# Kernel optimization log

Measured on AMD Instinct MI355X. Metric: run time of the kernel, lower is better.

Reference implementation:

```python
import jax, jax.numpy as jnp
import numpy as np

FILTER_SIZE = 256          # nperseg and conv kernel length
REG = 1e-7
B, C, T = 512, 8, 6000


def welch_psd(x, nperseg):
    # x: [B, C, T]; window=None (rect), fs=1, noverlap=nperseg//2, detrend by segment mean
    noverlap = nperseg // 2
    step = nperseg - noverlap
    num_seg = (x.shape[-1] - noverlap) // step
    idx = jnp.arange(nperseg)[None, :] + step * jnp.arange(num_seg)[:, None]  # [S, nperseg]
    seg = x[..., idx]                                   # [B, C, S, nperseg]
    seg = seg - seg.mean(axis=-1, keepdims=True)
    fft = jnp.fft.rfft(seg, axis=-1)                    # [B, C, S, F]
    psd = jnp.abs(fft) ** 2 / float(nperseg)
    # one-sided scaling: double all bins except DC (and Nyquist for even nperseg)
    if nperseg % 2 == 0:
        psd = psd.at[..., 1:-1].multiply(2.0)
    else:
        psd = psd.at[..., 1:].multiply(2.0)
    return psd.mean(axis=-2)                            # [B, C, F]


def setup_inputs() -> dict:
    key = jax.random.key(0)
    x = jax.random.normal(key, (B, C, T), dtype=jnp.float32)
    return {"x": x}


def reference(x):
    K = FILTER_SIZE
    n_chan = x.shape[1]
    # center
    x = x - x.mean(axis=-1, keepdims=True)
    psd = welch_psd(x, K) + REG                         # [B, C, F]
    F = psd.shape[-1]
    # barycenter (training, first_iter=True): weights = 1/F elementwise, sum over batch, squared; detached
    new_bary = jnp.sum(jnp.sqrt(psd) / F, axis=0) ** 2  # [C, F]
    target = jax.lax.stop_gradient(new_bary)
    # whitening/mapping filter in frequency domain
    D = jnp.sqrt(target)[None] / jnp.sqrt(psd)          # [B, C, F]
    H = jnp.fft.irfft(D, n=K, axis=-1)                  # [B, C, K]
    H = jnp.fft.fftshift(H, axes=-1)
    H = jnp.flip(H, axis=-1)
    # per-sample depthwise conv1d, padding='same' (torch: left=(K-1)//2, right=K//2 for stride 1)
    lp = (K - 1) // 2
    rp = (K - 1) - lp
    def dw(xb, hb):  # xb: [C, T], hb: [C, K]
        return jax.lax.conv_general_dilated(
            xb[None], hb[:, None, :], (1,), [(lp, rp)],
            feature_group_count=n_chan,
            dimension_numbers=("NCH", "OIH", "NCH"))[0]
    return jax.vmap(dw)(x, H)                           # [B, C, T]
```

## Files before the change

### kernel.cpp

```cpp
#include <hip/hip_runtime.h>
#include <math.h>

#define T_LEN 6000
#define NROWS 4096
#define NCH 8
#define F_BINS 129
#define CF (NCH*F_BINS)
#define NSLOT 16
#define REG_EPS 1e-7f

typedef _Float16 half8 __attribute__((ext_vector_type(8)));
typedef _Float16 half4_t __attribute__((ext_vector_type(4)));
typedef float f32x4 __attribute__((ext_vector_type(4)));

#define PSD_ROWS 8
__global__ __launch_bounds__(512, 2) void psd_kernel(const float* __restrict__ x,
                                                     float* __restrict__ psd,
                                                     float* __restrict__ means,
                                                     float* __restrict__ ssumN) {
  int tid = threadIdx.x;
  int lane = tid & 63;
  int w = tid >> 6;
  int l15 = lane & 15, l4 = lane >> 4;
  __shared__ __align__(16) _Float16 xh[2][6272];
  __shared__ float colsum[256];
  __shared__ float rowm[3][8];

  half8 bf[2][8];
  #pragma unroll
  for (int i = 0; i < 2; ++i) {
    int n = 16 * (2 * w + i) + l15;
    int nn = (n < 129) ? n : (n - 128);
    for (int kk = 0; kk < 8; ++kk) {
      half8 hb;
      for (int e = 0; e < 8; ++e) {
        int k = 32 * kk + 8 * l4 + e;
        float ang = (float)((nn * k) & 255) * (6.283185307179586f / 256.f);
        float s, c;
        __sincosf(ang, &s, &c);
        hb[e] = (_Float16)((n < 129) ? c : s);
      }
      bf[i][kk] = hb;
    }
  }

  int r0 = blockIdx.x * PSD_ROWS;
  float* myslot = ssumN + (size_t)(blockIdx.x & (NSLOT - 1)) * CF;
  float4 v[4];
  {
    const float* xr = x + (size_t)r0 * T_LEN;
    #pragma unroll
    for (int j = 0; j < 4; ++j) {
      int c = tid + 512 * j;
      v[j] = (c < 1500) ? ((const float4*)xr)[c] : make_float4(0.f, 0.f, 0.f, 0.f);
    }
    float rs = 0.f;
    #pragma unroll
    for (int j = 0; j < 4; ++j) {
      int c = tid + 512 * j;
      if (c < 1568) {
        float4 q = v[j];
        rs += q.x + q.y + q.z + q.w;
        half4_t h = { (_Float16)q.x, (_Float16)q.y, (_Float16)q.z, (_Float16)q.w };
        int byte = 8 * c;
        byte ^= ((byte >> 8) & 7) << 4;
        *(half4_t*)((char*)xh[0] + byte) = h;
      }
    }
    #pragma unroll
    for (int off = 32; off >= 1; off >>= 1) rs += __shfl_xor(rs, off);
    if (lane == 0) rowm[0][w] = rs;
    const float* x1 = x + (size_t)(r0 + 1) * T_LEN;
    #pragma unroll
    for (int j = 0; j < 4; ++j) {
      int c = tid + 512 * j;
      v[j] = (c < 1500) ? ((const float4*)x1)[c] : make_float4(0.f, 0.f, 0.f, 0.f);
    }
  }
  __syncthreads();

  for (int jr = 0; jr < PSD_ROWS; ++jr) {
    int r = r0 + jr;
    const char* xcur = (const char*)xh[jr & 1];
    if (jr + 1 < PSD_ROWS) {
      char* xnxt = (char*)xh[(jr + 1) & 1];
      float rs = 0.f;
      #pragma unroll
      for (int j = 0; j < 4; ++j) {
        int c = tid + 512 * j;
        if (c < 1568) {
          float4 q = v[j];
          rs += q.x + q.y + q.z + q.w;
          half4_t h = { (_Float16)q.x, (_Float16)q.y, (_Float16)q.z, (_Float16)q.w };
          int byte = 8 * c;
          byte ^= ((byte >> 8) & 7) << 4;
          *(half4_t*)(xnxt + byte) = h;
        }
      }
      if (jr + 2 < PSD_ROWS) {
        const float* xn = x + (size_t)(r + 2) * T_LEN;
        #pragma unroll
        for (int j = 0; j < 4; ++j) {
          int c = tid + 512 * j;
          v[j] = (c < 1500) ? ((const float4*)xn)[c] : make_float4(0.f, 0.f, 0.f, 0.f);
        }
      }
      #pragma unroll
      for (int off = 32; off >= 1; off >>= 1) rs += __shfl_xor(rs, off);
      if (lane == 0) rowm[(jr + 1) % 3][w] = rs;
    }
    f32x4 acc[2][3];
    #pragma unroll
    for (int i = 0; i < 2; ++i)
      #pragma unroll
      for (int mt = 0; mt < 3; ++mt)
        acc[i][mt] = (f32x4){0.f, 0.f, 0.f, 0.f};
    #pragma unroll
    for (int kk = 0; kk < 8; ++kk) {
      half8 a[3];
      #pragma unroll
      for (int mt = 0; mt < 3; ++mt) {
        int ab = 4096 * mt + 256 * l15 + 64 * kk + 16 * l4;
        ab ^= ((ab >> 8) & 7) << 4;
        a[mt] = *(const half8*)(xcur + ab);
      }
      #pragma unroll
      for (int mt = 0; mt < 3; ++mt) {
        acc[0][mt] = __builtin_amdgcn_mfma_f32_16x16x32_f16(a[mt], bf[0][kk], acc[0][mt], 0, 0, 0);
        acc[1][mt] = __builtin_amdgcn_mfma_f32_16x16x32_f16(a[mt], bf[1][kk], acc[1][mt], 0, 0, 0);
      }
    }
    float s0, s1;
    #pragma unroll
    for (int i = 0; i < 2; ++i) {
      float t = 0.f;
      #pragma unroll
      for (int j = 0; j < 4; ++j) {
        t += acc[i][0][j] * acc[i][0][j];
        t += acc[i][1][j] * acc[i][1][j];
        if (4 * l4 + j < 13) t += acc[i][2][j] * acc[i][2][j];
      }
      t += __shfl_xor(t, 16);
      t += __shfl_xor(t, 32);
      if (i == 0) s0 = t; else s1 = t;
    }
    __syncthreads();
    if (l4 == 0) {
      colsum[16 * (2 * w + 0) + l15] = s0;
      colsum[16 * (2 * w + 1) + l15] = s1;
    }
    __syncthreads();
    if (tid < F_BINS) {
      float vv;
      if (tid == 0) vv = 0.f;
      else if (tid == 128) vv = colsum[128] * (1.f / 11520.f);
      else vv = (colsum[tid] + colsum[tid + 128]) * (1.f / 5760.f);
      float p = vv + REG_EPS;
      psd[(size_t)r * F_BINS + tid] = p;
      atomicAdd(&myslot[jr * F_BINS + tid], sqrtf(p) * (1.f / (float)F_BINS));
    }
    if (tid == 0) {
      float ms = 0.f;
      #pragma unroll
      for (int q = 0; q < 8; ++q) ms += rowm[jr % 3][q];
      means[r] = ms * (1.f / (float)T_LEN);
    }
  }
}

#define BSTRIDE 296
__global__ __launch_bounds__(512) void conv_kernel(const float* __restrict__ x,
                                                   const float* __restrict__ means,
                                                   const float* __restrict__ psd,
                                                   const float* __restrict__ ssumN,
                                                   float* __restrict__ y) {
  int rc = blockIdx.x;
  int c = rc & (NCH - 1);
  int tid = threadIdx.x;
  int lane = tid & 63;
  int w = tid >> 6;
  __shared__ __align__(16) char smem[24576];
  _Float16* xh = (_Float16*)smem;
  _Float16* Bp = (_Float16*)(smem + 13056);
  float* part = (float*)(smem + 13056);
  float* dv = (float*)(smem + 22528);
  float* hv = (float*)(smem + 23044);
  const float* xr = x + (size_t)rc * T_LEN;
  float mean = means[rc];
  if (tid < F_BINS) {
    float s = 0.f;
    #pragma unroll
    for (int p = 0; p < NSLOT; ++p)
      s += ssumN[(size_t)p * CF + c * F_BINS + tid];
    dv[tid] = s * rsqrtf(psd[(size_t)rc * F_BINS + tid]);
  }
  #pragma unroll
  for (int j = 0; j < 4; ++j) {
    int q = tid + 512 * j;
    if (q < 1632) {
      int cc = q - 32;
      half4_t h;
      if (cc >= 0 && cc < 1500) {
        float4 vv = ((const float4*)xr)[cc];
        h = (half4_t){ (_Float16)(vv.x - mean), (_Float16)(vv.y - mean),
                       (_Float16)(vv.z - mean), (_Float16)(vv.w - mean) };
      } else {
        h = (half4_t){ (_Float16)0.f, (_Float16)0.f, (_Float16)0.f, (_Float16)0.f };
      }
      *(half4_t*)((char*)xh + 8 * q) = h;
    }
  }
  __syncthreads();
  if (tid < 258) {
    int t = tid >> 1, p = tid & 1;
    int k0 = p ? 64 : 1;
    int nk = p ? 64 : 63;
    float stc, sts;
    __sincosf((float)t * (6.283185307179586f / 256.f), &sts, &stc);
    float cr, ci;
    __sincosf((float)((t * k0) & 255) * (6.283185307179586f / 256.f), &ci, &cr);
    float acc = 0.f;
    for (int q = 0; q < nk; ++q) {
      acc = fmaf(dv[k0 + q], cr, acc);
      float nr = cr * stc - ci * sts;
      ci = cr * sts + ci * stc;
      cr = nr;
    }
    part[tid] = acc;
  }
  __syncthreads();
  if (tid < F_BINS) {
    float val = dv[0] + ((tid & 1) ? -dv[128] : dv[128]) +
                2.f * (part[2 * tid] + part[2 * tid + 1]);
    hv[tid] = val * (1.f / 256.f);
  }
  __syncthreads();
  #pragma unroll
  for (int j = 0; j < 3; ++j) {
    int idx = tid + 512 * j;
    if (idx < 1152) {
      int n = idx & 15;
      int qq = idx >> 4;
      int s0 = 4 * qq - n - 1;
      half4_t h;
      #pragma unroll
      for (int e = 0; e < 4; ++e) {
        int s = s0 + e;
        float hvv = 0.f;
        if (s >= 0 && s < 256) {
          int ii = s - 127; if (ii < 0) ii = -ii;
          hvv = hv[ii];
        }
        h[e] = (_Float16)hvv;
      }
      *(half4_t*)((char*)Bp + (size_t)n * (2 * BSTRIDE) + 8 * qq) = h;
    }
  }
  __syncthreads();

  int l15 = lane & 15, l4 = lane >> 4;
  f32x4 acc0 = {0.f,0.f,0.f,0.f}, acc1 = {0.f,0.f,0.f,0.f}, acc2 = {0.f,0.f,0.f,0.f};
  const _Float16* bbase = &Bp[BSTRIDE * l15 + 8 * l4];
  const _Float16* abase = &xh[16 * l15 + 8 * l4 + 768 * w];
  #pragma unroll
  for (int kk = 0; kk < 9; ++kk) {
    half8 b = *(const half8*)(bbase + 32 * kk);
    half8 a0 = *(const half8*)(abase + 32 * kk);
    half8 a1 = *(const half8*)(abase + 256 + 32 * kk);
    half8 a2 = *(const half8*)(abase + 512 + 32 * kk);
    acc0 = __builtin_amdgcn_mfma_f32_16x16x32_f16(a0, b, acc0, 0, 0, 0);
    acc1 = __builtin_amdgcn_mfma_f32_16x16x32_f16(a1, b, acc1, 0, 0, 0);
    acc2 = __builtin_amdgcn_mfma_f32_16x16x32_f16(a2, b, acc2, 0, 0, 0);
  }
  __syncthreads();
  float* bw = (float*)smem + 768 * w;
  #pragma unroll
  for (int i = 0; i < 3; ++i) {
    f32x4 a = (i == 0) ? acc0 : (i == 1) ? acc1 : acc2;
    #pragma unroll
    for (int j = 0; j < 4; ++j)
      bw[256 * i + 64 * l4 + 16 * j + l15] = a[j];
  }
  float* yr = y + (size_t)rc * T_LEN + 768 * w;
  const float4* b4 = (const float4*)bw;
  #pragma unroll
  for (int cc = 0; cc < 3; ++cc) {
    int fi = 768 * w + 256 * cc + 4 * lane;
    if (fi < T_LEN)
      *(float4*)&yr[256 * cc + 4 * lane] = b4[64 * cc + lane];
  }
}

extern "C" void kernel_launch(void* const* d_in, const int* in_sizes, int n_in,
                              void* d_out, int out_size, void* d_ws, size_t ws_size,
                              hipStream_t stream) {
  const float* x = (const float*)d_in[0];
  float* out = (float*)d_out;
  float* psd   = (float*)d_ws;
  float* ssumN = psd + (size_t)NROWS * F_BINS;
  float* means = ssumN + (size_t)NSLOT * CF;
  hipMemsetAsync(ssumN, 0, (size_t)NSLOT * CF * sizeof(float), stream);
  psd_kernel<<<NROWS / PSD_ROWS, 512, 0, stream>>>(x, psd, means, ssumN);
  conv_kernel<<<NROWS, 512, 0, stream>>>(x, means, psd, ssumN, out);
}
```

Baseline: 96.95 us.

## Precompute DFT basis in separate kernel and process one row per PSD block

A small new kernel builds the fp16 DFT basis once into workspace, and psd_kernel loads it from global memory instead of computing sincos per block. psd_kernel now runs one row per block (4096 blocks) with no double-buffered prefetch, in place of 8 rows per block with software pipelining. The aim is more parallelism across CUs and no repeated basis setup, at the cost of an extra launch, less intra-block overlap of loads with MFMA, and more per-block basis loads.

```diff
diff --git a/kernel.cpp b/kernel.cpp
--- a/kernel.cpp
+++ b/kernel.cpp
@@ -13,158 +13,122 @@
 typedef _Float16 half4_t __attribute__((ext_vector_type(4)));
 typedef float f32x4 __attribute__((ext_vector_type(4)));
 
-#define PSD_ROWS 8
-__global__ __launch_bounds__(512, 2) void psd_kernel(const float* __restrict__ x,
-                                                     float* __restrict__ psd,
-                                                     float* __restrict__ means,
-                                                     float* __restrict__ ssumN) {
+__global__ __launch_bounds__(256) void basis_kernel(_Float16* __restrict__ Bf) {
+  int g = blockIdx.x * 256 + threadIdx.x;
+  int lane = g & 63;
+  int ntkk = g >> 6;
+  int nt = ntkk >> 3, kk = ntkk & 7;
+  int n = 16 * nt + (lane & 15);
+  int k0 = 32 * kk + 8 * (lane >> 4);
+  half8 out;
+  #pragma unroll
+  for (int e = 0; e < 8; ++e) {
+    int k = k0 + e;
+    int m = (n < 129) ? ((n * k) & 255) : (((n - 128) * k) & 255);
+    float ang = (float)m * (6.283185307179586f / 256.f);
+    float v = (n < 129) ? cosf(ang) : sinf(ang);
+    out[e] = (_Float16)v;
+  }
+  *(half8*)(Bf + (size_t)g * 8) = out;
+}
+
+__global__ __launch_bounds__(512) void psd_kernel(const float* __restrict__ x,
+                                                  const _Float16* __restrict__ Bf,
+                                                  float* __restrict__ psd,
+                                                  float* __restrict__ means,
+                                                  float* __restrict__ ssumN) {
   int tid = threadIdx.x;
   int lane = tid & 63;
   int w = tid >> 6;
   int l15 = lane & 15, l4 = lane >> 4;
-  __shared__ __align__(16) _Float16 xh[2][6272];
+  __shared__ __align__(16) _Float16 xh[6272];
   __shared__ float colsum[256];
-  __shared__ float rowm[3][8];
+  __shared__ float rowm[8];
+  int r = blockIdx.x;
 
   half8 bf[2][8];
   #pragma unroll
   for (int i = 0; i < 2; ++i) {
-    int n = 16 * (2 * w + i) + l15;
-    int nn = (n < 129) ? n : (n - 128);
-    for (int kk = 0; kk < 8; ++kk) {
-      half8 hb;
-      for (int e = 0; e < 8; ++e) {
-        int k = 32 * kk + 8 * l4 + e;
-        float ang = (float)((nn * k) & 255) * (6.283185307179586f / 256.f);
-        float s, c;
-        __sincosf(ang, &s, &c);
-        hb[e] = (_Float16)((n < 129) ? c : s);
-      }
-      bf[i][kk] = hb;
-    }
-  }
-
-  int r0 = blockIdx.x * PSD_ROWS;
-  float* myslot = ssumN + (size_t)(blockIdx.x & (NSLOT - 1)) * CF;
-  float4 v[4];
-  {
-    const float* xr = x + (size_t)r0 * T_LEN;
+    const _Float16* bb = Bf + (size_t)(((2 * w + i) * 8) * 64 + lane) * 8;
+    #pragma unroll
+    for (int kk = 0; kk < 8; ++kk)
+      bf[i][kk] = *(const half8*)(bb + (size_t)kk * 512);
+  }
+
+  const float* xr = x + (size_t)r * T_LEN;
+  float rs = 0.f;
+  #pragma unroll
+  for (int j = 0; j < 4; ++j) {
+    int c = tid + 512 * j;
+    if (c < 1568) {
+      float4 q = (c < 1500) ? ((const float4*)xr)[c] : make_float4(0.f, 0.f, 0.f, 0.f);
+      rs += q.x + q.y + q.z + q.w;
+      half4_t h = { (_Float16)q.x, (_Float16)q.y, (_Float16)q.z, (_Float16)q.w };
+      int byte = 8 * c;
+      byte ^= ((byte >> 8) & 7) << 4;
+      *(half4_t*)((char*)xh + byte) = h;
+    }
+  }
+  #pragma unroll
+  for (int off = 32; off >= 1; off >>= 1) rs += __shfl_xor(rs, off);
+  if (lane == 0) rowm[w] = rs;
+  __syncthreads();
+
+  f32x4 acc[2][3];
+  #pragma unroll
+  for (int i = 0; i < 2; ++i)
+    #pragma unroll
+    for (int mt = 0; mt < 3; ++mt)
+      acc[i][mt] = (f32x4){0.f, 0.f, 0.f, 0.f};
+  #pragma unroll
+  for (int kk = 0; kk < 8; ++kk) {
+    half8 a[3];
+    #pragma unroll
+    for (int mt = 0; mt < 3; ++mt) {
+      int ab = 4096 * mt + 256 * l15 + 64 * kk + 16 * l4;
+      ab ^= ((ab >> 8) & 7) << 4;
+      a[mt] = *(const half8*)((const char*)xh + ab);
+    }
+    #pragma unroll
+    for (int mt = 0; mt < 3; ++mt) {
+      acc[0][mt] = __builtin_amdgcn_mfma_f32_16x16x32_f16(a[mt], bf[0][kk], acc[0][mt], 0, 0, 0);
+      acc[1][mt] = __builtin_amdgcn_mfma_f32_16x16x32_f16(a[mt], bf[1][kk], acc[1][mt], 0, 0, 0);
+    }
+  }
+  float s0, s1;
+  #pragma unroll
+  for (int i = 0; i < 2; ++i) {
+    float t = 0.f;
     #pragma unroll
     for (int j = 0; j < 4; ++j) {
-      int c = tid + 512 * j;
-      v[j] = (c < 1500) ? ((const float4*)xr)[c] : make_float4(0.f, 0.f, 0.f, 0.f);
-    }
-    float rs = 0.f;
-    #pragma unroll
-    for (int j = 0; j < 4; ++j) {
-      int c = tid + 512 * j;
-      if (c < 1568) {
-        float4 q = v[j];
-        rs += q.x + q.y + q.z + q.w;
-        half4_t h = { (_Float16)q.x, (_Float16)q.y, (_Float16)q.z, (_Float16)q.w };
-        int byte = 8 * c;
-        byte ^= ((byte >> 8) & 7) << 4;
-        *(half4_t*)((char*)xh[0] + byte) = h;
-      }
-    }
-    #pragma unroll
-    for (int off = 32; off >= 1; off >>= 1) rs += __shfl_xor(rs, off);
-    if (lane == 0) rowm[0][w] = rs;
-    const float* x1 = x + (size_t)(r0 + 1) * T_LEN;
-    #pragma unroll
-    for (int j = 0; j < 4; ++j) {
-      int c = tid + 512 * j;
-      v[j] = (c < 1500) ? ((const float4*)x1)[c] : make_float4(0.f, 0.f, 0.f, 0.f);
-    }
-  }
-  __syncthreads();
-
-  for (int jr = 0; jr < PSD_ROWS; ++jr) {
-    int r = r0 + jr;
-    const char* xcur = (const char*)xh[jr & 1];
-    if (jr + 1 < PSD_ROWS) {
-      char* xnxt = (char*)xh[(jr + 1) & 1];
-      float rs = 0.f;
-      #pragma unroll
-      for (int j = 0; j < 4; ++j) {
-        int c = tid + 512 * j;
-        if (c < 1568) {
-          float4 q = v[j];
-          rs += q.x + q.y + q.z + q.w;
-          half4_t h = { (_Float16)q.x, (_Float16)q.y, (_Float16)q.z, (_Float16)q.w };
-          int byte = 8 * c;
-          byte ^= ((byte >> 8) & 7) << 4;
-          *(half4_t*)(xnxt + byte) = h;
-        }
-      }
-      if (jr + 2 < PSD_ROWS) {
-        const float* xn = x + (size_t)(r + 2) * T_LEN;
-        #pragma unroll
-        for (int j = 0; j < 4; ++j) {
-          int c = tid + 512 * j;
-          v[j] = (c < 1500) ? ((const float4*)xn)[c] : make_float4(0.f, 0.f, 0.f, 0.f);
-        }
-      }
-      #pragma unroll
-      for (int off = 32; off >= 1; off >>= 1) rs += __shfl_xor(rs, off);
-      if (lane == 0) rowm[(jr + 1) % 3][w] = rs;
-    }
-    f32x4 acc[2][3];
-    #pragma unroll
-    for (int i = 0; i < 2; ++i)
-      #pragma unroll
-      for (int mt = 0; mt < 3; ++mt)
-        acc[i][mt] = (f32x4){0.f, 0.f, 0.f, 0.f};
-    #pragma unroll
-    for (int kk = 0; kk < 8; ++kk) {
-      half8 a[3];
-      #pragma unroll
-      for (int mt = 0; mt < 3; ++mt) {
-        int ab = 4096 * mt + 256 * l15 + 64 * kk + 16 * l4;
-        ab ^= ((ab >> 8) & 7) << 4;
-        a[mt] = *(const half8*)(xcur + ab);
-      }
-      #pragma unroll
-      for (int mt = 0; mt < 3; ++mt) {
-        acc[0][mt] = __builtin_amdgcn_mfma_f32_16x16x32_f16(a[mt], bf[0][kk], acc[0][mt], 0, 0, 0);
-        acc[1][mt] = __builtin_amdgcn_mfma_f32_16x16x32_f16(a[mt], bf[1][kk], acc[1][mt], 0, 0, 0);
-      }
-    }
-    float s0, s1;
-    #pragma unroll
-    for (int i = 0; i < 2; ++i) {
-      float t = 0.f;
-      #pragma unroll
-      for (int j = 0; j < 4; ++j) {
-        t += acc[i][0][j] * acc[i][0][j];
-        t += acc[i][1][j] * acc[i][1][j];
-        if (4 * l4 + j < 13) t += acc[i][2][j] * acc[i][2][j];
-      }
-      t += __shfl_xor(t, 16);
-      t += __shfl_xor(t, 32);
-      if (i == 0) s0 = t; else s1 = t;
-    }
-    __syncthreads();
-    if (l4 == 0) {
-      colsum[16 * (2 * w + 0) + l15] = s0;
-      colsum[16 * (2 * w + 1) + l15] = s1;
-    }
-    __syncthreads();
-    if (tid < F_BINS) {
-      float vv;
-      if (tid == 0) vv = 0.f;
-      else if (tid == 128) vv = colsum[128] * (1.f / 11520.f);
-      else vv = (colsum[tid] + colsum[tid + 128]) * (1.f / 5760.f);
-      float p = vv + REG_EPS;
-      psd[(size_t)r * F_BINS + tid] = p;
-      atomicAdd(&myslot[jr * F_BINS + tid], sqrtf(p) * (1.f / (float)F_BINS));
-    }
-    if (tid == 0) {
-      float ms = 0.f;
-      #pragma unroll
-      for (int q = 0; q < 8; ++q) ms += rowm[jr % 3][q];
-      means[r] = ms * (1.f / (float)T_LEN);
-    }
+      t += acc[i][0][j] * acc[i][0][j];
+      t += acc[i][1][j] * acc[i][1][j];
+      if (4 * l4 + j < 13) t += acc[i][2][j] * acc[i][2][j];
+    }
+    t += __shfl_xor(t, 16);
+    t += __shfl_xor(t, 32);
+    if (i == 0) s0 = t; else s1 = t;
+  }
+  if (l4 == 0) {
+    colsum[16 * (2 * w + 0) + l15] = s0;
+    colsum[16 * (2 * w + 1) + l15] = s1;
+  }
+  __syncthreads();
+  if (tid < F_BINS) {
+    float vv;
+    if (tid == 0) vv = 0.f;
+    else if (tid == 128) vv = colsum[128] * (1.f / 11520.f);
+    else vv = (colsum[tid] + colsum[tid + 128]) * (1.f / 5760.f);
+    float p = vv + REG_EPS;
+    psd[(size_t)r * F_BINS + tid] = p;
+    atomicAdd(&ssumN[(size_t)((r >> 3) & (NSLOT - 1)) * CF + (r & 7) * F_BINS + tid],
+              sqrtf(p) * (1.f / (float)F_BINS));
+  }
+  if (tid == 0) {
+    float ms = 0.f;
+    #pragma unroll
+    for (int q = 0; q < 8; ++q) ms += rowm[q];
+    means[r] = ms * (1.f / (float)T_LEN);
   }
 }
 
@@ -299,7 +263,9 @@
   float* psd   = (float*)d_ws;
   float* ssumN = psd + (size_t)NROWS * F_BINS;
   float* means = ssumN + (size_t)NSLOT * CF;
+  _Float16* Bf = (_Float16*)(means + NROWS);
   hipMemsetAsync(ssumN, 0, (size_t)NSLOT * CF * sizeof(float), stream);
-  psd_kernel<<<NROWS / PSD_ROWS, 512, 0, stream>>>(x, psd, means, ssumN);
+  basis_kernel<<<32, 256, 0, stream>>>(Bf);
+  psd_kernel<<<NROWS, 512, 0, stream>>>(x, Bf, psd, means, ssumN);
   conv_kernel<<<NROWS, 512, 0, stream>>>(x, means, psd, ssumN, out);
 }
```

New measurement: 96.70 us. About the same (-0.3%).
